# Performance work log

Measured on AMD Instinct MI355X. Metric: run time of the kernel, lower is better.

The kernel has to match this reference:

```python
import jax, jax.numpy as jnp
import numpy as np

B, N, CIN, C = 2, 400000, 192, 128
Y, X, Z = 512, 512, 40
EPS1 = 1e-5   # default BatchNorm1d eps for feature_proj
EPS2 = 1e-3   # norm_fn eps=0.001 for shared_conv BN


def setup_inputs() -> dict:
    key = jax.random.key(0)
    ks = jax.random.split(key, 12)
    voxel_features = jax.random.normal(ks[0], (N, CIN), jnp.float32)
    bi = jax.random.randint(ks[1], (N,), 0, B)
    zi = jax.random.randint(ks[2], (N,), 0, Z)
    yi = jax.random.randint(ks[3], (N,), 0, Y)
    xi = jax.random.randint(ks[4], (N,), 0, X)
    voxel_coords = jnp.stack([bi, zi, yi, xi], axis=1).astype(jnp.int32)  # (N,4)=[b,z,y,x]
    # feature_proj: Linear(CIN->C) + BN1d (inference stats) + ReLU
    W_proj = jax.random.normal(ks[5], (CIN, C), jnp.float32) * np.float32(1.0 / np.sqrt(CIN))
    b_proj = jnp.zeros((C,), jnp.float32)
    bn1_gamma = jnp.ones((C,), jnp.float32)
    bn1_beta = jnp.zeros((C,), jnp.float32)
    bn1_mean = jax.random.normal(ks[6], (C,), jnp.float32) * np.float32(0.1)
    bn1_var = jax.random.uniform(ks[7], (C,), jnp.float32, 0.5, 1.5)
    # shared_conv: SubMConv2d(C,C,3,pad=1,bias) + BN(eps=1e-3) + ReLU
    conv_w = jax.random.normal(ks[8], (3, 3, C, C), jnp.float32) * np.float32(1.0 / np.sqrt(9 * C))
    conv_b = jnp.zeros((C,), jnp.float32)
    bn2_gamma = jnp.ones((C,), jnp.float32)
    bn2_beta = jnp.zeros((C,), jnp.float32)
    bn2_mean = jax.random.normal(ks[9], (C,), jnp.float32) * np.float32(0.1)
    bn2_var = jax.random.uniform(ks[10], (C,), jnp.float32, 0.5, 1.5)
    return dict(voxel_features=voxel_features, voxel_coords=voxel_coords,
                W_proj=W_proj, b_proj=b_proj,
                bn1_gamma=bn1_gamma, bn1_beta=bn1_beta, bn1_mean=bn1_mean, bn1_var=bn1_var,
                conv_w=conv_w, conv_b=conv_b,
                bn2_gamma=bn2_gamma, bn2_beta=bn2_beta, bn2_mean=bn2_mean, bn2_var=bn2_var)


def reference(voxel_features, voxel_coords, W_proj, b_proj,
              bn1_gamma, bn1_beta, bn1_mean, bn1_var,
              conv_w, conv_b, bn2_gamma, bn2_beta, bn2_mean, bn2_var):
    # 1) feature_proj (Linear + BN1d inference + ReLU)
    f = voxel_features @ W_proj + b_proj                      # (N, C)
    f = (f - bn1_mean) * jax.lax.rsqrt(bn1_var + EPS1) * bn1_gamma + bn1_beta
    f = jax.nn.relu(f)
    # 2) bev_aggregate: unique([b,y,x]) + index_add == scatter-sum to dense BEV grid
    bi, yi, xi = voxel_coords[:, 0], voxel_coords[:, 2], voxel_coords[:, 3]
    dense = jnp.zeros((B, Y, X, C), f.dtype).at[bi, yi, xi].add(f)
    active = jnp.zeros((B, Y, X), bool).at[bi, yi, xi].set(True)
    # 3) SubMConv2d(3x3, pad=1) + BN + ReLU; subm == dense conv masked to active sites
    out = jax.lax.conv_general_dilated(dense, conv_w, (1, 1), 'SAME',
                                       dimension_numbers=('NHWC', 'HWIO', 'NHWC')) + conv_b
    out = (out - bn2_mean) * jax.lax.rsqrt(bn2_var + EPS2) * bn2_gamma + bn2_beta
    out = jax.nn.relu(out)
    # sparse tensor only holds active sites; zero elsewhere
    return jnp.where(active[..., None], out, jnp.float32(0.0))  # (B, Y, X, C)
```

## Files before the change

### kernel.cpp

```cpp
#include <hip/hip_runtime.h>

#define Bq 2
#define Yq 512
#define Xq 512
#define NVOX 400000

typedef __bf16 bf16x8 __attribute__((ext_vector_type(8)));
typedef float f32x4 __attribute__((ext_vector_type(4)));
typedef float f32x16 __attribute__((ext_vector_type(16)));
typedef short s16x8 __attribute__((ext_vector_type(8)));
typedef short s16x2 __attribute__((ext_vector_type(2)));

__device__ __forceinline__ short f2bf_s(float f){
    return __builtin_bit_cast(short, static_cast<__bf16>(f));
}

__device__ __forceinline__ void atomic_pk_add_bf16(short* addr, unsigned data){
#if __has_builtin(__builtin_amdgcn_global_atomic_fadd_v2bf16)
    s16x2 v; v[0] = (short)(data & 0xffff); v[1] = (short)(data >> 16);
    __builtin_amdgcn_global_atomic_fadd_v2bf16(
        (__attribute__((address_space(1))) s16x2*)addr, v);
#else
    asm volatile("global_atomic_pk_add_bf16 %0, %1, off"
                 :: "v"(addr), "v"(data) : "memory");
#endif
}

__global__ void kprep(const float* __restrict__ conv_w, const float* __restrict__ W_proj,
                      short* __restrict__ wTs, short* __restrict__ wpT){
    int tid = blockIdx.x*256 + threadIdx.x;
    if (tid < 9*128*128){
        int tap = tid >> 14; int r = tid & 16383; int co = r >> 7; int ci = r & 127;
        int g = ci >> 3, e = ci & 7;
        wTs[tap*16384 + co*128 + (((g & 8) | ((g & 7) ^ (co & 7))) << 3) + e] =
            f2bf_s(conv_w[tap*16384 + ci*128 + co]);
    }
    int e = tid - 9*128*128;
    if (e >= 0 && e < 128*192){
        int co = e / 192; int ci = e - co*192;
        wpT[e] = f2bf_s(W_proj[ci*128 + co]);
    }
}

__global__ void kcount(const int* __restrict__ vc, unsigned* __restrict__ cnt,
                       unsigned char* __restrict__ act){
    int i = blockIdx.x*256 + threadIdx.x;
    if (i >= NVOX) return;
    const int4 c = *reinterpret_cast<const int4*>(vc + i*4);
    int cell = (c.x*Yq + c.z)*Xq + c.w;
    act[cell] = 1;
    atomicAdd(&cnt[cell], 1u);
}

__global__ void __launch_bounds__(256, 2)
kproj(const float* __restrict__ vf, const int* __restrict__ vc,
      const unsigned* __restrict__ cnt,
      const short* __restrict__ wpT, const float* __restrict__ bp,
      const float* __restrict__ g1, const float* __restrict__ be1,
      const float* __restrict__ mu1, const float* __restrict__ va1,
      short* __restrict__ dbf){
    __shared__ short A[64*200];
    __shared__ int cellsPk[64];
    const int t = threadIdx.x;
    const int v0 = blockIdx.x * 64;

    const float4* vf4 = reinterpret_cast<const float4*>(vf);
    #pragma unroll
    for (int j = 0; j < 12; ++j){
        int i = t + j*256;
        int v = i / 48, kq = i - v*48;
        float4 x = vf4[(size_t)(v0 + v)*48 + kq];
        short4 s; s.x=f2bf_s(x.x); s.y=f2bf_s(x.y); s.z=f2bf_s(x.z); s.w=f2bf_s(x.w);
        *reinterpret_cast<short4*>(&A[v*200 + kq*4]) = s;
    }
    if (t < 64){
        int vi = v0 + t;
        int bi = vc[vi*4 + 0], yi = vc[vi*4 + 2], xi = vc[vi*4 + 3];
        unsigned cn = cnt[(bi*Yq + yi)*Xq + xi];
        int P = (bi*514 + (yi + 1))*514 + (xi + 1);
        cellsPk[t] = (P*8 + ((xi + 1) & 7)) | ((cn > 1) ? (1 << 30) : 0);
    }
    __syncthreads();

    const int w  = t >> 6;
    const int l  = t & 63;
    const int lr = l & 15;
    const int q  = l >> 4;

    const short* wp_lane = wpT + (size_t)(w*32 + lr)*192 + q*8;
    bf16x8 bb[2][6];
    #pragma unroll
    for (int n = 0; n < 2; ++n)
        #pragma unroll
        for (int kc = 0; kc < 6; ++kc)
            bb[n][kc] = *reinterpret_cast<const bf16x8*>(wp_lane + n*16*192 + kc*32);

    f32x4 acc[4][2] = {};
    #pragma unroll
    for (int kc = 0; kc < 6; ++kc){
        bf16x8 a[4];
        #pragma unroll
        for (int m = 0; m < 4; ++m)
            a[m] = *reinterpret_cast<const bf16x8*>(&A[(m*16 + lr)*200 + kc*32 + q*8]);
        #pragma unroll
        for (int m = 0; m < 4; ++m)
            #pragma unroll
            for (int n = 0; n < 2; ++n)
                acc[m][n] = __builtin_amdgcn_mfma_f32_16x16x32_bf16(a[m], bb[n][kc], acc[m][n], 0, 0, 0);
    }

    #pragma unroll
    for (int n = 0; n < 2; ++n){
        int c = w*32 + n*16 + lr;
        float s1  = g1[c] * rsqrtf(va1[c] + 1e-5f);
        float sh1 = be1[c] + (bp[c] - mu1[c]) * s1;
        #pragma unroll
        for (int m = 0; m < 4; ++m){
            #pragma unroll
            for (int r = 0; r < 4; ++r){
                int vx = m*16 + q*4 + r;
                float val = fmaxf(fmaf(acc[m][n][r], s1, sh1), 0.f);
                float vp  = __shfl_xor(val, 1);
                if ((lr & 1) == 0){
                    int pk = cellsPk[vx];
                    int multi = pk >> 30;
                    int P = (pk & 0x3fffffff) >> 3, xp7 = pk & 7;
                    short* addr = dbf + (size_t)P*128 + (((c >> 3) ^ xp7) << 3) + (c & 7);
                    unsigned data = (unsigned)(unsigned short)f2bf_s(val)
                                  | ((unsigned)(unsigned short)f2bf_s(vp) << 16);
                    if (!multi){
                        if (data) *reinterpret_cast<unsigned*>(addr) = data;
                    } else {
                        if (data) atomic_pk_add_bf16(addr, data);
                    }
                }
            }
        }
    }
}

__global__ void __launch_bounds__(512, 2)
kconv(const short* __restrict__ dbf, const short* __restrict__ wTs,
      const unsigned char* __restrict__ act, const float* __restrict__ cb,
      const float* __restrict__ g2, const float* __restrict__ be2,
      const float* __restrict__ mu2, const float* __restrict__ va2,
      float* __restrict__ out){
    __shared__ short Atile[6*1056*8];
    __shared__ short Bbuf[2][1024*8];
    const int t = threadIdx.x;
    const int bid = (blockIdx.x & 7)*256 + (blockIdx.x >> 3);
    const int b   = bid >> 10;
    const int rem = bid & 1023;
    const int y0  = (rem >> 3) << 2;
    const int x0  = (rem & 7) << 6;

    const int w   = t >> 6, l = t & 63;
    const int yy  = w >> 1, nn = w & 1;
    const int l31 = l & 31, hi = l >> 5;
    const int wbase16 = w*64*16;

    #define STAGE_B(BUF, H) do {                                              \
        const short* gb = wTs + (size_t)((H) >> 1)*16384 + ((H) & 1)*64;      \
        _Pragma("unroll")                                                     \
        for (int j = 0; j < 2; ++j){                                          \
            int S = j*512 + t;                                                \
            const short* gp = gb + (S >> 3)*128 + (S & 7)*8;                  \
            __builtin_amdgcn_global_load_lds(                                 \
                (const __attribute__((address_space(1))) void*)gp,            \
                (__attribute__((address_space(3))) void*)                    \
                    ((char*)Bbuf[BUF] + (size_t)(j*512*16) + wbase16), 16, 0, 0); \
        }                                                                     \
    } while(0)

    STAGE_B(0, 0);
    #pragma unroll
    for (int j = 0; j < 13; ++j){
        int S = j*512 + t;
        if (S < 6336){
            int r = S / 1056, s = S - r*1056;
            const short* gp = dbf + ((size_t)((b*514 + (y0 + r))*514 + x0)*16 + s)*8;
            __builtin_amdgcn_global_load_lds(
                (const __attribute__((address_space(1))) void*)gp,
                (__attribute__((address_space(3))) void*)
                    ((char*)Atile + (size_t)(j*512*16) + wbase16), 16, 0, 0);
        }
    }

    f32x16 acc[2][2] = {};
    const int bReadBase = (nn*64 + l31)*64;
    const int bXor = l31 & 7;

    #pragma unroll
    for (int h = 0; h < 18; ++h){
        asm volatile("s_waitcnt vmcnt(0)" ::: "memory");
        __builtin_amdgcn_s_barrier();
        __builtin_amdgcn_sched_barrier(0);
        if (h < 17) STAGE_B((h+1) & 1, h+1);
        const short* Bc = Bbuf[h & 1];
        const int tap = h >> 1, hh = h & 1;
        const int ky = tap / 3, kx = tap - ky*3;
        const int row = yy + ky;
        const int p0 = l31 + kx, p1 = p0 + 32;
        const int base0 = (row*1056 + p0*16)*8;
        const int base1 = (row*1056 + p1*16)*8;
        const int pk7 = p0 & 7;
        #pragma unroll
        for (int kc = 0; kc < 4; ++kc){
            const int ks  = kc*2 + hi;
            const int q   = ((hh*8 + ks) ^ pk7) << 3;
            const int qb  = (ks ^ bXor) << 3;
            bf16x8 a0 = *reinterpret_cast<const bf16x8*>(&Atile[base0 + q]);
            bf16x8 a1 = *reinterpret_cast<const bf16x8*>(&Atile[base1 + q]);
            bf16x8 b0 = *reinterpret_cast<const bf16x8*>(&Bc[bReadBase + qb]);
            bf16x8 b1 = *reinterpret_cast<const bf16x8*>(&Bc[bReadBase + 2048 + qb]);
            acc[0][0] = __builtin_amdgcn_mfma_f32_32x32x16_bf16(a0, b0, acc[0][0], 0, 0, 0);
            acc[0][1] = __builtin_amdgcn_mfma_f32_32x32x16_bf16(a0, b1, acc[0][1], 0, 0, 0);
            acc[1][0] = __builtin_amdgcn_mfma_f32_32x32x16_bf16(a1, b0, acc[1][0], 0, 0, 0);
            acc[1][1] = __builtin_amdgcn_mfma_f32_32x32x16_bf16(a1, b1, acc[1][1], 0, 0, 0);
        }
    }
    #undef STAGE_B

    const int yg = y0 + yy;
    const size_t rowcell = (size_t)(b*Yq + yg)*Xq + x0;
    #pragma unroll
    for (int ni = 0; ni < 2; ++ni){
        int c = nn*64 + ni*32 + l31;
        float s2  = g2[c] * rsqrtf(va2[c] + 1e-3f);
        float sh2 = be2[c] + (cb[c] - mu2[c]) * s2;
        #pragma unroll
        for (int mi = 0; mi < 2; ++mi){
            #pragma unroll
            for (int r = 0; r < 16; ++r){
                int pos = mi*32 + (r & 3) + ((r >> 2) << 3) + hi*4;
                size_t cell = rowcell + pos;
                float v = act[cell] ? fmaxf(fmaf(acc[mi][ni][r], s2, sh2), 0.f) : 0.f;
                out[cell*128 + c] = v;
            }
        }
    }
}

extern "C" void kernel_launch(void* const* d_in, const int* in_sizes, int n_in,
                              void* d_out, int out_size, void* d_ws, size_t ws_size,
                              hipStream_t stream){
    const float* vf  = (const float*)d_in[0];
    const int*   vc  = (const int*)  d_in[1];
    const float* Wp  = (const float*)d_in[2];
    const float* bp  = (const float*)d_in[3];
    const float* g1  = (const float*)d_in[4];
    const float* be1 = (const float*)d_in[5];
    const float* mu1 = (const float*)d_in[6];
    const float* va1 = (const float*)d_in[7];
    const float* cw  = (const float*)d_in[8];
    const float* cb  = (const float*)d_in[9];
    const float* g2  = (const float*)d_in[10];
    const float* be2 = (const float*)d_in[11];
    const float* mu2 = (const float*)d_in[12];
    const float* va2 = (const float*)d_in[13];
    float* out = (float*)d_out;
    char* ws = (char*)d_ws;

    if (ws_size < 138233856ull) return;
    short* dbf = (short*)ws;
    unsigned char* act = (unsigned char*)(ws + 135268352);
    short* wTs = (short*)(ws + 135792640);
    short* wpT = (short*)(ws + 136087552);
    unsigned* cnt = (unsigned*)(ws + 136136704);

    hipMemsetAsync(dbf, 0, 135268352, stream);
    hipMemsetAsync(act, 0, 524288, stream);
    hipMemsetAsync(cnt, 0, 2097152, stream);
    kprep<<<672, 256, 0, stream>>>(cw, Wp, wTs, wpT);
    kcount<<<1563, 256, 0, stream>>>(vc, cnt, act);
    kproj<<<6250, 256, 0, stream>>>(vf, vc, cnt, wpT, bp, g1, be1, mu1, va1, dbf);
    kconv<<<2048, 512, 0, stream>>>(dbf, wTs, act, cb, g2, be2, mu2, va2, out);
}
```

Measured before the change: 390.6 us.

## Stream conv halo rows, balance proj stores across lanes, raise occupancy, setprio MFMA

kconv's A-tile prologue now loads only the first four halo rows. The last two rows are fetched inside the first two iterations of the tap loop, so their latency overlaps the early MFMAs and the start of compute is no longer delayed. The MFMA group is wrapped in s_setprio to favour math waves. kproj raises its occupancy hint to four blocks per CU and spreads the packed bf16 stores over both even and odd lanes according to m, so twice as many lanes issue stores at a time. The changes carry register-pressure risk in kproj and some ordering risk, since the late rows are only needed from tap row 1 onward and rely on the vmcnt wait at the barrier.

```diff
diff --git a/kernel.cpp b/kernel.cpp
--- a/kernel.cpp
+++ b/kernel.cpp
@@ -52,7 +52,7 @@
     atomicAdd(&cnt[cell], 1u);
 }
 
-__global__ void __launch_bounds__(256, 2)
+__global__ void __launch_bounds__(256, 4)
 kproj(const float* __restrict__ vf, const int* __restrict__ vc,
       const unsigned* __restrict__ cnt,
       const short* __restrict__ wpT, const float* __restrict__ bp,
@@ -109,11 +109,13 @@
                 acc[m][n] = __builtin_amdgcn_mfma_f32_16x16x32_bf16(a[m], bb[n][kc], acc[m][n], 0, 0, 0);
     }
 
+    const int odd = lr & 1;
     #pragma unroll
     for (int n = 0; n < 2; ++n){
         int c = w*32 + n*16 + lr;
         float s1  = g1[c] * rsqrtf(va1[c] + 1e-5f);
         float sh1 = be1[c] + (bp[c] - mu1[c]) * s1;
+        int cpair = c - odd;
         #pragma unroll
         for (int m = 0; m < 4; ++m){
             #pragma unroll
@@ -121,17 +123,19 @@
                 int vx = m*16 + q*4 + r;
                 float val = fmaxf(fmaf(acc[m][n][r], s1, sh1), 0.f);
                 float vp  = __shfl_xor(val, 1);
-                if ((lr & 1) == 0){
+                if (odd == (m >> 1)){
                     int pk = cellsPk[vx];
                     int multi = pk >> 30;
                     int P = (pk & 0x3fffffff) >> 3, xp7 = pk & 7;
-                    short* addr = dbf + (size_t)P*128 + (((c >> 3) ^ xp7) << 3) + (c & 7);
-                    unsigned data = (unsigned)(unsigned short)f2bf_s(val)
-                                  | ((unsigned)(unsigned short)f2bf_s(vp) << 16);
-                    if (!multi){
-                        if (data) *reinterpret_cast<unsigned*>(addr) = data;
-                    } else {
-                        if (data) atomic_pk_add_bf16(addr, data);
+                    short* addr = dbf + (size_t)P*128 + (((cpair >> 3) ^ xp7) << 3) + (cpair & 7);
+                    unsigned lo = odd ? (unsigned)(unsigned short)f2bf_s(vp)
+                                      : (unsigned)(unsigned short)f2bf_s(val);
+                    unsigned hi = odd ? (unsigned)(unsigned short)f2bf_s(val)
+                                      : (unsigned)(unsigned short)f2bf_s(vp);
+                    unsigned data = lo | (hi << 16);
+                    if (data){
+                        if (!multi) *reinterpret_cast<unsigned*>(addr) = data;
+                        else atomic_pk_add_bf16(addr, data);
                     }
                 }
             }
@@ -174,9 +178,9 @@
 
     STAGE_B(0, 0);
     #pragma unroll
-    for (int j = 0; j < 13; ++j){
+    for (int j = 0; j < 9; ++j){
         int S = j*512 + t;
-        if (S < 6336){
+        if (S < 4224){
             int r = S / 1056, s = S - r*1056;
             const short* gp = dbf + ((size_t)((b*514 + (y0 + r))*514 + x0)*16 + s)*8;
             __builtin_amdgcn_global_load_lds(
@@ -196,6 +200,21 @@
         __builtin_amdgcn_s_barrier();
         __builtin_amdgcn_sched_barrier(0);
         if (h < 17) STAGE_B((h+1) & 1, h+1);
+        if (h < 2){
+            const int rr = 4 + h;
+            #pragma unroll
+            for (int j = 0; j < 3; ++j){
+                int S = j*512 + t;
+                if (S < 1056){
+                    const short* gp = dbf + ((size_t)((b*514 + (y0 + rr))*514 + x0)*16 + S)*8;
+                    __builtin_amdgcn_global_load_lds(
+                        (const __attribute__((address_space(1))) void*)gp,
+                        (__attribute__((address_space(3))) void*)
+                            ((char*)Atile + (size_t)(rr*1056 + j*512 + w*64)*16), 16, 0, 0);
+                }
+            }
+        }
+        __builtin_amdgcn_sched_barrier(0);
         const short* Bc = Bbuf[h & 1];
         const int tap = h >> 1, hh = h & 1;
         const int ky = tap / 3, kx = tap - ky*3;
@@ -213,10 +232,12 @@
             bf16x8 a1 = *reinterpret_cast<const bf16x8*>(&Atile[base1 + q]);
             bf16x8 b0 = *reinterpret_cast<const bf16x8*>(&Bc[bReadBase + qb]);
             bf16x8 b1 = *reinterpret_cast<const bf16x8*>(&Bc[bReadBase + 2048 + qb]);
+            __builtin_amdgcn_s_setprio(1);
             acc[0][0] = __builtin_amdgcn_mfma_f32_32x32x16_bf16(a0, b0, acc[0][0], 0, 0, 0);
             acc[0][1] = __builtin_amdgcn_mfma_f32_32x32x16_bf16(a0, b1, acc[0][1], 0, 0, 0);
             acc[1][0] = __builtin_amdgcn_mfma_f32_32x32x16_bf16(a1, b0, acc[1][0], 0, 0, 0);
             acc[1][1] = __builtin_amdgcn_mfma_f32_32x32x16_bf16(a1, b1, acc[1][1], 0, 0, 0);
+            __builtin_amdgcn_s_setprio(0);
         }
     }
     #undef STAGE_B
```

Measured after the change: 399.5 us. +2.3%, slower.
